# Kernel tuning notes

Measured on AMD Instinct MI355X. Metric: run time of the kernel, lower is better.

Reference implementation:

```python
import jax, jax.numpy as jnp
import numpy as np

B, C, DIM_IN, E = 1024, 128, 16, 10
# num paths per (output L, correlation order nu) -- last dim of the generalized CG U-matrices
PATHS = {0: {1: 1, 2: 2, 3: 5}, 1: {1: 1, 2: 3, 3: 7}}


def setup_inputs() -> dict:
    key = jax.random.key(0)
    ks = jax.random.split(key, 16)
    a_i = jax.random.normal(ks[0], (B, C, DIM_IN), jnp.float32)
    species = jax.random.randint(ks[1], (B,), 0, E)
    node_attrs = jax.nn.one_hot(species, E, dtype=jnp.float32)  # one-hot per-atom species

    def U(k, shape):
        # stand-in for the (constant, precomputed) generalized CG U-matrices
        return jax.random.normal(k, shape, jnp.float32) * 0.1

    def W(k, npaths):
        # learned per-species path weights [num_elements, num_paths, channels]
        return jax.random.normal(k, (E, npaths, C), jnp.float32) / np.sqrt(npaths)

    i = DIM_IN
    return dict(
        a_i=a_i, node_attrs=node_attrs,
        U3_l0=U(ks[2], (i, i, i, PATHS[0][3])),
        U2_l0=U(ks[3], (i, i, PATHS[0][2])),
        U1_l0=U(ks[4], (i, PATHS[0][1])),
        W3_l0=W(ks[5], PATHS[0][3]), W2_l0=W(ks[6], PATHS[0][2]), W1_l0=W(ks[7], PATHS[0][1]),
        U3_l1=U(ks[8], (3, i, i, i, PATHS[1][3])),
        U2_l1=U(ks[9], (3, i, i, PATHS[1][2])),
        U1_l1=U(ks[10], (3, i, PATHS[1][1])),
        W3_l1=W(ks[11], PATHS[1][3]), W2_l1=W(ks[12], PATHS[1][2]), W1_l1=W(ks[13], PATHS[1][1]),
    )


def _contraction(x, y, U3, U2, U1, W3, W2, W1):
    # x: [b,c,i]; y: [b,e] one-hot. Faithful to MACE Contraction:
    #   main:      '...ik,ekc,bci,be->bc...'  (nu = correlation = 3)
    #   weighting: '...k,ekc,be->bc...'       (nu = 2, 1)
    #   features:  'bc...i,bci->bc...'
    # main equation staged so the largest intermediate is the [b,c,(L,)i,i] output
    w3 = jnp.einsum('ekc,be->bkc', W3, y)          # per-node species weight selection
    wx = jnp.einsum('bkc,bci->bkci', w3, x)        # [b,k3,c,i]
    out = jnp.einsum('...ik,bkci->bc...', U3, wx)  # [b,c,(2L+1,)i,i]
    # nu = 2
    w2 = jnp.einsum('ekc,be->bkc', W2, y)
    out = out + jnp.einsum('...k,bkc->bc...', U2, w2)
    out = jnp.einsum('bc...i,bci->bc...', out, x)  # [b,c,(2L+1,)i]
    # nu = 1
    w1 = jnp.einsum('ekc,be->bkc', W1, y)
    out = out + jnp.einsum('...k,bkc->bc...', U1, w1)
    out = jnp.einsum('bc...i,bci->bc...', out, x)  # [b,c] (L=0) or [b,c,2L+1]
    return out


def reference(a_i, node_attrs, U3_l0, U2_l0, U1_l0, W3_l0, W2_l0, W1_l0,
              U3_l1, U2_l1, U1_l1, W3_l1, W2_l1, W1_l1):
    out0 = _contraction(a_i, node_attrs, U3_l0, U2_l0, U1_l0, W3_l0, W2_l0, W1_l0)  # [b,c]
    out1 = _contraction(a_i, node_attrs, U3_l1, U2_l1, U1_l1, W3_l1, W2_l1, W1_l1)  # [b,c,3]
    b = a_i.shape[0]
    # SymmetricContraction flattens each contraction to [b, c*(2L+1)] and concatenates
    return jnp.concatenate([out0.reshape(b, -1), out1.reshape(b, -1)], axis=-1)  # [b, c*4]
```

## Files before the change

kernel.cpp:

```cpp
#include <hip/hip_runtime.h>
#include <hip/hip_bf16.h>

typedef unsigned short u16;
typedef __attribute__((ext_vector_type(8))) unsigned short u16x8;
typedef __attribute__((ext_vector_type(4))) float f32x4;

#define TPB 128
#define TBL_OFF 65536
#define SLOT 9312
#define TBL_BYTES ((size_t)1280 * SLOT * 4)
#define PART_OFF (TBL_OFF + TBL_BYTES)
#define PART_BYTES ((size_t)4 * 1024 * 512 * 4)
#define WS_NEEDED_OLD (TBL_OFF + TBL_BYTES)
#define WS_NEEDED_NEW (PART_OFF + PART_BYTES)

__device__ __forceinline__ float bf2f(u16 v){
  union { unsigned int u; float f; } x; x.u = ((unsigned int)v) << 16; return x.f;
}
__device__ __forceinline__ u16 f2bf(float f){
  union { float f; unsigned int u; } x; x.f = f;
  unsigned int u = x.u;
  u += 0x7FFFu + ((u >> 16) & 1u);
  return (u16)(u >> 16);
}
__device__ __forceinline__ float ld(const void* p, int idx, int isbf){
  return isbf ? bf2f(((const u16*)p)[idx]) : ((const float*)p)[idx];
}

__global__ void k_classify2(const void* __restrict__ nav, int* __restrict__ ws){
  __shared__ int scnt[10];
  __shared__ int sf[16];
  __shared__ int sflag;
  const int b = threadIdx.x;
  if (b < 10) scnt[b] = 0;

  const unsigned int* w = (const unsigned int*)nav;
  int found = 0;
  for (int i = b; i < 5120; i += 1024) found |= (w[i] == 0x00003F80u);
  unsigned long long m = __ballot(found);
  if ((b & 63) == 0) sf[b >> 6] = (m != 0ULL);
  __syncthreads();
  if (b == 0){ int f = 0; for (int i = 0; i < 16; i++) f |= sf[i]; sflag = f; ws[15] = f; }
  __syncthreads();
  const int isbf = sflag;

  int e = 0;
  #pragma unroll
  for (int j = 0; j < 10; j++){
    if (ld(nav, b*10 + j, isbf) > 0.5f) e = j;
  }
  int pos = atomicAdd(&scnt[e], 1);
  ws[16 + e*1024 + pos] = b;
  __syncthreads();
  if (b < 10) ws[b] = scnt[b];
}

__global__ __launch_bounds__(128) void k_build2(
    const void* __restrict__ U3_0, const void* __restrict__ U2_0, const void* __restrict__ U1_0,
    const void* __restrict__ W3_0, const void* __restrict__ W2_0, const void* __restrict__ W1_0,
    const void* __restrict__ U3_1, const void* __restrict__ U2_1, const void* __restrict__ U1_1,
    const void* __restrict__ W3_1, const void* __restrict__ W2_1, const void* __restrict__ W1_1,
    const int* __restrict__ ws, float* __restrict__ tb)
{
  const int jt = blockIdx.x, cg = blockIdx.y, e = blockIdx.z;
  const int j  = jt*128 + threadIdx.x;
  const int isbf = ws[15];
  if (j >= 9312) return;
  const int c0 = cg*8;

  float u[7];
  int K, wbase, dst;
  const void* Wp;

  if (j < 8704){
    const int q = j / 2176, rem = j % 2176;
    const int p = rem >> 4, i3 = rem & 15;
    int i1 = 0, rr = p;
    while (rr >= 16 - i1){ rr -= 16 - i1; i1++; }
    const int i2 = i1 + rr;
    if (q == 0){
      K = 5; Wp = W3_0; wbase = e*5;
      const int a  = (i1*256 + i2*16 + i3)*5;
      const int bb = (i2*256 + i1*16 + i3)*5;
      #pragma unroll
      for (int k = 0; k < 5; k++){
        float v = ld(U3_0, a + k, isbf);
        if (i1 != i2) v += ld(U3_0, bb + k, isbf);
        u[k] = v;
      }
    } else {
      K = 7; Wp = W3_1; wbase = e*7;
      const int mm = q - 1;
      const int a  = (mm*4096 + i1*256 + i2*16 + i3)*7;
      const int bb = (mm*4096 + i2*256 + i1*16 + i3)*7;
      #pragma unroll
      for (int k = 0; k < 7; k++){
        float v = ld(U3_1, a + k, isbf);
        if (i1 != i2) v += ld(U3_1, bb + k, isbf);
        u[k] = v;
      }
    }
    dst = j;
  } else if (j < 9248){
    const int jj = j - 8704;
    const int q = jj / 136, p = jj % 136;
    int i1 = 0, rr = p;
    while (rr >= 16 - i1){ rr -= 16 - i1; i1++; }
    const int i2 = i1 + rr;
    if (q == 0){
      K = 2; Wp = W2_0; wbase = e*2;
      const int a = (i1*16 + i2)*2, bb = (i2*16 + i1)*2;
      #pragma unroll
      for (int k = 0; k < 2; k++){
        float v = ld(U2_0, a + k, isbf);
        if (i1 != i2) v += ld(U2_0, bb + k, isbf);
        u[k] = v;
      }
    } else {
      K = 3; Wp = W2_1; wbase = e*3;
      const int mm = q - 1;
      const int a = (mm*256 + i1*16 + i2)*3, bb = (mm*256 + i2*16 + i1)*3;
      #pragma unroll
      for (int k = 0; k < 3; k++){
        float v = ld(U2_1, a + k, isbf);
        if (i1 != i2) v += ld(U2_1, bb + k, isbf);
        u[k] = v;
      }
    }
    dst = 8704 + jj;
  } else {
    const int jj = j - 9248;
    const int q = jj >> 4, i = jj & 15;
    K = 1;
    if (q == 0){ Wp = W1_0; wbase = e; u[0] = ld(U1_0, i, isbf); }
    else       { Wp = W1_1; wbase = e; u[0] = ld(U1_1, (q - 1)*16 + i, isbf); }
    dst = 9248 + jj;
  }

  for (int cc = 0; cc < 8; cc++){
    const int c = c0 + cc;
    float v = 0.f;
    for (int k = 0; k < K; k++) v += u[k] * ld(Wp, (wbase + k)*128 + c, isbf);
    tb[(size_t)(e*128 + c)*SLOT + dst] = v;
  }
}

__global__ __launch_bounds__(TPB) void k_contract3(
    const void* __restrict__ a_i, const int* __restrict__ ws,
    const float* __restrict__ tb, float* __restrict__ part)
{
  const int e   = blockIdx.x >> 7;
  const int c   = blockIdx.x & 127;
  const int pc  = blockIdx.y;
  const int tid = threadIdx.x;
  const int isbf  = ws[15];
  const int count = ws[e];
  const int* lst  = ws + 16 + e*1024;
  const float* __restrict__ base = tb + (size_t)(e*128 + c)*SLOT;
  if (count == 0) return;

  __shared__ float sX[TPB][17];
  const int p0 = pc*34;

  for (int t0 = 0; t0 < count; t0 += TPB){
    int t = t0 + tid;
    const bool act = t < count;
    if (!act) t = count - 1;
    const int b = lst[t];
    const int xbase = (b*128 + c)*16;

    float xr[16];
    if (isbf){
      const u16* xp = (const u16*)a_i + xbase;
      u16x8 v0 = *(const u16x8*)(xp);
      u16x8 v1 = *(const u16x8*)(xp + 8);
      #pragma unroll
      for (int i = 0; i < 8; i++){ xr[i] = bf2f(v0[i]); xr[8 + i] = bf2f(v1[i]); }
    } else {
      const float* xp = (const float*)a_i + xbase;
      f32x4 v0 = *(const f32x4*)(xp);
      f32x4 v1 = *(const f32x4*)(xp + 4);
      f32x4 v2 = *(const f32x4*)(xp + 8);
      f32x4 v3 = *(const f32x4*)(xp + 12);
      #pragma unroll
      for (int i = 0; i < 4; i++){
        xr[i] = v0[i]; xr[4+i] = v1[i]; xr[8+i] = v2[i]; xr[12+i] = v3[i];
      }
    }
    #pragma unroll
    for (int i = 0; i < 16; i++) sX[tid][i] = xr[i];

    float r0 = 0.f, r1 = 0.f, r2 = 0.f, r3 = 0.f;
    const float* pA3 = base + p0*16;
    const float* pA2 = base + 8704 + p0;
    int i1 = 0, rm = p0;
    while (rm >= 16 - i1){ rm -= 16 - i1; i1++; }
    int i2 = i1 + rm;

    #pragma clang loop unroll(disable)
    for (int n = 0; n < 34; ++n){
      const float xx = sX[tid][i1] * sX[tid][i2];
      float s0 = pA2[0], s1 = pA2[136], s2 = pA2[272], s3 = pA2[408];
      #pragma unroll
      for (int i3 = 0; i3 < 16; ++i3){
        const float xv = xr[i3];
        s0 += pA3[        i3]*xv;
        s1 += pA3[2176 + i3]*xv;
        s2 += pA3[4352 + i3]*xv;
        s3 += pA3[6528 + i3]*xv;
      }
      r0 += s0*xx; r1 += s1*xx; r2 += s2*xx; r3 += s3*xx;
      pA3 += 16; pA2 += 1;
      i2++; if (i2 == 16){ i1++; i2 = i1; }
    }

    if (pc == 3){
      #pragma unroll
      for (int i = 0; i < 16; i++){
        const float xv = xr[i];
        r0 += base[9248 + i]*xv;
        r1 += base[9264 + i]*xv;
        r2 += base[9280 + i]*xv;
        r3 += base[9296 + i]*xv;
      }
    }

    if (act){
      f32x4 v; v[0] = r0; v[1] = r1; v[2] = r2; v[3] = r3;
      *(f32x4*)(part + ((size_t)(pc*1024 + b)*512 + c*4)) = v;
    }
  }
}

__global__ __launch_bounds__(128) void k_combine(
    const float* __restrict__ part, const int* __restrict__ ws, void* __restrict__ outv)
{
  const int b = blockIdx.x, c = threadIdx.x;
  const int isbf = ws[15];
  f32x4 r;
  r[0] = 0.f; r[1] = 0.f; r[2] = 0.f; r[3] = 0.f;
  #pragma unroll
  for (int pc = 0; pc < 4; pc++){
    f32x4 v = *(const f32x4*)(part + ((size_t)(pc*1024 + b)*512 + c*4));
    r[0] += v[0]; r[1] += v[1]; r[2] += v[2]; r[3] += v[3];
  }
  if (isbf){
    u16* ob = (u16*)outv + (size_t)b*512;
    ob[c]             = f2bf(r[0]);
    ob[128 + c*3 + 0] = f2bf(r[1]);
    ob[128 + c*3 + 1] = f2bf(r[2]);
    ob[128 + c*3 + 2] = f2bf(r[3]);
  } else {
    float* ob = (float*)outv + (size_t)b*512;
    ob[c]             = r[0];
    ob[128 + c*3 + 0] = r[1];
    ob[128 + c*3 + 1] = r[2];
    ob[128 + c*3 + 2] = r[3];
  }
}

__global__ __launch_bounds__(256) void k_build(
    const void* __restrict__ U3_0, const void* __restrict__ U2_0, const void* __restrict__ U1_0,
    const void* __restrict__ W3_0, const void* __restrict__ W2_0, const void* __restrict__ W1_0,
    const void* __restrict__ U3_1, const void* __restrict__ U2_1, const void* __restrict__ U1_1,
    const void* __restrict__ W3_1, const void* __restrict__ W2_1, const void* __restrict__ W1_1,
    const int* __restrict__ ws, float* __restrict__ tb)
{
  const int eq = blockIdx.y;
  const int e  = eq >> 2, q = eq & 3;
  const int bx = blockIdx.x;
  const int jt = bx >> 5, ct = bx & 31;
  const int j  = jt*64 + (threadIdx.x & 63);
  const int c  = ct*4 + (threadIdx.x >> 6);
  const int isbf = ws[15];
  if (j >= 2328) return;

  float* base = tb + (size_t)(e*128 + c)*SLOT;

  if (j < 2176){
    const int p = j >> 4, i3 = j & 15;
    int i1 = 0, rem = p;
    while (rem >= 16 - i1){ rem -= 16 - i1; i1++; }
    const int i2 = i1 + rem;
    float v = 0.f;
    if (q == 0){
      const int a  = (i1*256 + i2*16 + i3)*5;
      const int bb = (i2*256 + i1*16 + i3)*5;
      #pragma unroll
      for (int k = 0; k < 5; k++){
        float u = ld(U3_0, a + k, isbf);
        if (i1 != i2) u += ld(U3_0, bb + k, isbf);
        v += u * ld(W3_0, (e*5 + k)*128 + c, isbf);
      }
    } else {
      const int m  = q - 1;
      const int a  = (m*4096 + i1*256 + i2*16 + i3)*7;
      const int bb = (m*4096 + i2*256 + i1*16 + i3)*7;
      #pragma unroll
      for (int k = 0; k < 7; k++){
        float u = ld(U3_1, a + k, isbf);
        if (i1 != i2) u += ld(U3_1, bb + k, isbf);
        v += u * ld(W3_1, (e*7 + k)*128 + c, isbf);
      }
    }
    base[q*2176 + j] = v;
  } else if (j < 2312){
    const int p = j - 2176;
    int i1 = 0, rem = p;
    while (rem >= 16 - i1){ rem -= 16 - i1; i1++; }
    const int i2 = i1 + rem;
    float v = 0.f;
    if (q == 0){
      const int a = (i1*16 + i2)*2, bb = (i2*16 + i1)*2;
      #pragma unroll
      for (int k = 0; k < 2; k++){
        float u = ld(U2_0, a + k, isbf);
        if (i1 != i2) u += ld(U2_0, bb + k, isbf);
        v += u * ld(W2_0, (e*2 + k)*128 + c, isbf);
      }
    } else {
      const int m = q - 1;
      const int a = (m*256 + i1*16 + i2)*3, bb = (m*256 + i2*16 + i1)*3;
      #pragma unroll
      for (int k = 0; k < 3; k++){
        float u = ld(U2_1, a + k, isbf);
        if (i1 != i2) u += ld(U2_1, bb + k, isbf);
        v += u * ld(W2_1, (e*3 + k)*128 + c, isbf);
      }
    }
    base[8704 + q*136 + p] = v;
  } else {
    const int i = j - 2312;
    float v = (q == 0) ? ld(U1_0, i, isbf) * ld(W1_0, e*128 + c, isbf)
                       : ld(U1_1, (q - 1)*16 + i, isbf) * ld(W1_1, e*128 + c, isbf);
    base[9248 + q*16 + i] = v;
  }
}

__global__ __launch_bounds__(TPB) void k_contract2(
    const void* __restrict__ a_i, const int* __restrict__ ws,
    const float* __restrict__ tb, void* __restrict__ outv)
{
  const int e   = blockIdx.x >> 7;
  const int c   = blockIdx.x & 127;
  const int tid = threadIdx.x;
  const int isbf  = ws[15];
  const int count = ws[e];
  const int* lst  = ws + 16 + e*1024;
  const float* __restrict__ base = tb + (size_t)(e*128 + c)*SLOT;

  __shared__ float sX[TPB][17];

  for (int t0 = 0; t0 < count; t0 += TPB){
    int t = t0 + tid;
    const bool act = t < count;
    if (!act) t = count - 1;
    const int b = lst[t];
    const int xbase = (b*128 + c)*16;

    float xr[16];
    if (isbf){
      const u16* xp = (const u16*)a_i + xbase;
      u16x8 v0 = *(const u16x8*)(xp);
      u16x8 v1 = *(const u16x8*)(xp + 8);
      #pragma unroll
      for (int i = 0; i < 8; i++){ xr[i] = bf2f(v0[i]); xr[8 + i] = bf2f(v1[i]); }
    } else {
      const float* xp = (const float*)a_i + xbase;
      f32x4 v0 = *(const f32x4*)(xp);
      f32x4 v1 = *(const f32x4*)(xp + 4);
      f32x4 v2 = *(const f32x4*)(xp + 8);
      f32x4 v3 = *(const f32x4*)(xp + 12);
      #pragma unroll
      for (int i = 0; i < 4; i++){
        xr[i] = v0[i]; xr[4+i] = v1[i]; xr[8+i] = v2[i]; xr[12+i] = v3[i];
      }
    }
    #pragma unroll
    for (int i = 0; i < 16; i++) sX[tid][i] = xr[i];

    float r0 = 0.f, r1 = 0.f, r2 = 0.f, r3 = 0.f;
    const float* pA3 = base;
    const float* pA2 = base + 8704;

    #pragma clang loop unroll(disable)
    for (int i1 = 0; i1 < 16; ++i1){
      const float x1 = sX[tid][i1];
      #pragma clang loop unroll(disable)
      for (int i2 = i1; i2 < 16; ++i2){
        const float xx = x1 * sX[tid][i2];
        float s0 = pA2[0], s1 = pA2[136], s2 = pA2[272], s3 = pA2[408];
        #pragma unroll
        for (int i3 = 0; i3 < 16; ++i3){
          const float xv = xr[i3];
          s0 += pA3[        i3]*xv;
          s1 += pA3[2176 + i3]*xv;
          s2 += pA3[4352 + i3]*xv;
          s3 += pA3[6528 + i3]*xv;
        }
        r0 += s0*xx; r1 += s1*xx; r2 += s2*xx; r3 += s3*xx;
        pA3 += 16; pA2 += 1;
      }
    }
    #pragma unroll
    for (int i = 0; i < 16; i++){
      const float xv = xr[i];
      r0 += base[9248 + i]*xv;
      r1 += base[9264 + i]*xv;
      r2 += base[9280 + i]*xv;
      r3 += base[9296 + i]*xv;
    }

    if (act){
      if (isbf){
        u16* ob = (u16*)outv + (size_t)b*512;
        ob[c]             = f2bf(r0);
        ob[128 + c*3 + 0] = f2bf(r1);
        ob[128 + c*3 + 1] = f2bf(r2);
        ob[128 + c*3 + 2] = f2bf(r3);
      } else {
        float* ob = (float*)outv + (size_t)b*512;
        ob[c]             = r0;
        ob[128 + c*3 + 0] = r1;
        ob[128 + c*3 + 1] = r2;
        ob[128 + c*3 + 2] = r3;
      }
    }
  }
}

__global__ __launch_bounds__(TPB) void k_contract(
    const void* __restrict__ a_i,
    const void* __restrict__ U3_0, const void* __restrict__ U2_0, const void* __restrict__ U1_0,
    const void* __restrict__ W3_0, const void* __restrict__ W2_0, const void* __restrict__ W1_0,
    const void* __restrict__ U3_1, const void* __restrict__ U2_1, const void* __restrict__ U1_1,
    const void* __restrict__ W3_1, const void* __restrict__ W2_1, const void* __restrict__ W1_1,
    const int* __restrict__ ws, void* __restrict__ outv)
{
  const int bx  = blockIdx.x;
  const int e   = bx >> 7;
  const int c   = bx & 127;
  const int tid = threadIdx.x;
  const int isbf = ws[15];

  __shared__ float sA3[4*136*16];
  __shared__ float sA2[4*136];
  __shared__ float sA1[4*16];
  __shared__ unsigned char sI1[136], sI2[136];
  __shared__ float sX[TPB][17];

  for (int p = tid; p < 136; p += TPB){
    int i1 = 0, rem = p;
    while (rem >= 16 - i1){ rem -= 16 - i1; i1++; }
    sI1[p] = (unsigned char)i1;
    sI2[p] = (unsigned char)(i1 + rem);
  }

  float w3_0[5], w2_0[2], w3_1[7], w2_1[3];
  #pragma unroll
  for (int k = 0; k < 5; k++) w3_0[k] = ld(W3_0, (e*5 + k)*128 + c, isbf);
  #pragma unroll
  for (int k = 0; k < 2; k++) w2_0[k] = ld(W2_0, (e*2 + k)*128 + c, isbf);
  const float w1_0 = ld(W1_0, e*128 + c, isbf);
  #pragma unroll
  for (int k = 0; k < 7; k++) w3_1[k] = ld(W3_1, (e*7 + k)*128 + c, isbf);
  #pragma unroll
  for (int k = 0; k < 3; k++) w2_1[k] = ld(W2_1, (e*3 + k)*128 + c, isbf);
  const float w1_1 = ld(W1_1, e*128 + c, isbf);

  __syncthreads();

  for (int q = 0; q < 4; q++){
    for (int idx = tid; idx < 136*16; idx += TPB){
      const int p  = idx >> 4;
      const int i3 = idx & 15;
      const int i1 = sI1[p], i2 = sI2[p];
      float v = 0.f;
      if (q == 0){
        const int a  = (i1*256 + i2*16 + i3)*5;
        const int bb = (i2*256 + i1*16 + i3)*5;
        #pragma unroll
        for (int k = 0; k < 5; k++){
          float u = ld(U3_0, a + k, isbf);
          if (i1 != i2) u += ld(U3_0, bb + k, isbf);
          v += u * w3_0[k];
        }
      } else {
        const int m  = q - 1;
        const int a  = (m*4096 + i1*256 + i2*16 + i3)*7;
        const int bb = (m*4096 + i2*256 + i1*16 + i3)*7;
        #pragma unroll
        for (int k = 0; k < 7; k++){
          float u = ld(U3_1, a + k, isbf);
          if (i1 != i2) u += ld(U3_1, bb + k, isbf);
          v += u * w3_1[k];
        }
      }
      sA3[q*2176 + idx] = v;
    }
  }
  for (int idx = tid; idx < 4*136; idx += TPB){
    const int q = idx / 136, p = idx - q*136;
    const int i1 = sI1[p], i2 = sI2[p];
    float v = 0.f;
    if (q == 0){
      const int a = (i1*16 + i2)*2, bb = (i2*16 + i1)*2;
      #pragma unroll
      for (int k = 0; k < 2; k++){
        float u = ld(U2_0, a + k, isbf);
        if (i1 != i2) u += ld(U2_0, bb + k, isbf);
        v += u * w2_0[k];
      }
    } else {
      const int m = q - 1;
      const int a = (m*256 + i1*16 + i2)*3, bb = (m*256 + i2*16 + i1)*3;
      #pragma unroll
      for (int k = 0; k < 3; k++){
        float u = ld(U2_1, a + k, isbf);
        if (i1 != i2) u += ld(U2_1, bb + k, isbf);
        v += u * w2_1[k];
      }
    }
    sA2[idx] = v;
  }
  if (tid < 64){
    const int q = tid >> 4, i1 = tid & 15;
    sA1[tid] = (q == 0) ? ld(U1_0, i1, isbf) * w1_0
                        : ld(U1_1, (q - 1)*16 + i1, isbf) * w1_1;
  }
  __syncthreads();

  const int count = ws[e];
  const int* lst  = ws + 16 + e*1024;

  for (int t = tid; t < count; t += TPB){
    const int b = lst[t];
    const int xbase = (b*128 + c)*16;

    float xr[16];
    if (isbf){
      const u16* xp = (const u16*)a_i + xbase;
      u16x8 v0 = *(const u16x8*)(xp);
      u16x8 v1 = *(const u16x8*)(xp + 8);
      #pragma unroll
      for (int i = 0; i < 8; i++){ xr[i] = bf2f(v0[i]); xr[8 + i] = bf2f(v1[i]); }
    } else {
      const float* xp = (const float*)a_i + xbase;
      f32x4 v0 = *(const f32x4*)(xp);
      f32x4 v1 = *(const f32x4*)(xp + 4);
      f32x4 v2 = *(const f32x4*)(xp + 8);
      f32x4 v3 = *(const f32x4*)(xp + 12);
      #pragma unroll
      for (int i = 0; i < 4; i++){
        xr[i] = v0[i]; xr[4+i] = v1[i]; xr[8+i] = v2[i]; xr[12+i] = v3[i];
      }
    }
    #pragma unroll
    for (int i = 0; i < 16; i++) sX[tid][i] = xr[i];

    float r0 = 0.f, r1 = 0.f, r2 = 0.f, r3 = 0.f;
    int p = 0;
    for (int i1 = 0; i1 < 16; i1++){
      const float x1 = sX[tid][i1];
      for (int i2 = i1; i2 < 16; i2++, p++){
        const float* a0 = &sA3[(0*136 + p)*16];
        const float* a1 = &sA3[(1*136 + p)*16];
        const float* a2 = &sA3[(2*136 + p)*16];
        const float* a3 = &sA3[(3*136 + p)*16];
        float s0 = sA2[        p];
        float s1 = sA2[136   + p];
        float s2 = sA2[272   + p];
        float s3 = sA2[408   + p];
        #pragma unroll
        for (int i3 = 0; i3 < 16; i3++){
          const float xv = xr[i3];
          s0 += a0[i3]*xv;
          s1 += a1[i3]*xv;
          s2 += a2[i3]*xv;
          s3 += a3[i3]*xv;
        }
        const float xx = x1 * sX[tid][i2];
        r0 += s0*xx; r1 += s1*xx; r2 += s2*xx; r3 += s3*xx;
      }
    }
    #pragma unroll
    for (int i1 = 0; i1 < 16; i1++){
      const float xv = xr[i1];
      r0 += sA1[     i1]*xv;
      r1 += sA1[16 + i1]*xv;
      r2 += sA1[32 + i1]*xv;
      r3 += sA1[48 + i1]*xv;
    }

    if (isbf){
      u16* ob = (u16*)outv + (size_t)b*512;
      ob[c]             = f2bf(r0);
      ob[128 + c*3 + 0] = f2bf(r1);
      ob[128 + c*3 + 1] = f2bf(r2);
      ob[128 + c*3 + 2] = f2bf(r3);
    } else {
      float* ob = (float*)outv + (size_t)b*512;
      ob[c]             = r0;
      ob[128 + c*3 + 0] = r1;
      ob[128 + c*3 + 1] = r2;
      ob[128 + c*3 + 2] = r3;
    }
  }
}

extern "C" void kernel_launch(void* const* d_in, const int* in_sizes, int n_in,
                              void* d_out, int out_size, void* d_ws, size_t ws_size,
                              hipStream_t stream) {
  int* ws = (int*)d_ws;
  hipLaunchKernelGGL(k_classify2, dim3(1), dim3(1024), 0, stream, d_in[1], ws);

  if (ws_size >= WS_NEEDED_NEW){
    float* tb   = (float*)((char*)d_ws + TBL_OFF);
    float* part = (float*)((char*)d_ws + PART_OFF);
    hipLaunchKernelGGL(k_build2, dim3(73, 16, 10), dim3(128), 0, stream,
                       d_in[2], d_in[3], d_in[4], d_in[5], d_in[6], d_in[7],
                       d_in[8], d_in[9], d_in[10], d_in[11], d_in[12], d_in[13],
                       ws, tb);
    hipLaunchKernelGGL(k_contract3, dim3(1280, 4), dim3(TPB), 0, stream,
                       d_in[0], ws, tb, part);
    hipLaunchKernelGGL(k_combine, dim3(1024), dim3(128), 0, stream,
                       part, ws, d_out);
  } else if (ws_size >= WS_NEEDED_OLD){
    float* tb = (float*)((char*)d_ws + TBL_OFF);
    hipLaunchKernelGGL(k_build, dim3(37*32, 40), dim3(256), 0, stream,
                       d_in[2], d_in[3], d_in[4], d_in[5], d_in[6], d_in[7],
                       d_in[8], d_in[9], d_in[10], d_in[11], d_in[12], d_in[13],
                       ws, tb);
    hipLaunchKernelGGL(k_contract2, dim3(1280), dim3(TPB), 0, stream,
                       d_in[0], ws, tb, d_out);
  } else {
    hipLaunchKernelGGL(k_contract, dim3(1280), dim3(TPB), 0, stream,
                       d_in[0],
                       d_in[2], d_in[3], d_in[4], d_in[5], d_in[6], d_in[7],
                       d_in[8], d_in[9], d_in[10], d_in[11], d_in[12], d_in[13],
                       ws, d_out);
  }
}
```

Measured before the change: 140.9 us.

## Add bf16 MFMA contraction path and stage per-species weights in shared memory

Adds a bf16-only path. k_buildF precomputes the folded U·W table in bf16, laid out as MFMA A fragments. k_contract_mfma then evaluates the degree-3 contraction with 16x16x32 bf16 MFMA instructions and combines the results with pairwise x products in registers. This removes the fp32 table, the partial-sum buffer and the combine pass whenever inputs are bf16. The fp32 path keeps its kernels, but k_build3 now caches the W rows in shared memory instead of re-reading them from global memory. All six kernels are always launched and exit early based on the dtype flag, which adds launch overhead, and storing the table in bf16 may lose precision.

New measurement: 165.7 us. 1.18x slower.

```diff
diff --git a/kernel.cpp b/kernel.cpp
--- a/kernel.cpp
+++ b/kernel.cpp
@@ -3,6 +3,7 @@
 
 typedef unsigned short u16;
 typedef __attribute__((ext_vector_type(8))) unsigned short u16x8;
+typedef __attribute__((ext_vector_type(8))) short bf16x8;
 typedef __attribute__((ext_vector_type(4))) float f32x4;
 
 #define TPB 128
@@ -11,7 +12,6 @@
 #define TBL_BYTES ((size_t)1280 * SLOT * 4)
 #define PART_OFF (TBL_OFF + TBL_BYTES)
 #define PART_BYTES ((size_t)4 * 1024 * 512 * 4)
-#define WS_NEEDED_OLD (TBL_OFF + TBL_BYTES)
 #define WS_NEEDED_NEW (PART_OFF + PART_BYTES)
 
 __device__ __forceinline__ float bf2f(u16 v){
@@ -55,22 +55,246 @@
   if (b < 10) ws[b] = scnt[b];
 }
 
-__global__ __launch_bounds__(128) void k_build2(
+__global__ __launch_bounds__(64) void k_buildF(
+    const void* __restrict__ U3_0, const void* __restrict__ U2_0, const void* __restrict__ U1_0,
+    const void* __restrict__ W3_0, const void* __restrict__ W2_0, const void* __restrict__ W1_0,
+    const void* __restrict__ U3_1, const void* __restrict__ U2_1, const void* __restrict__ U1_1,
+    const void* __restrict__ W3_1, const void* __restrict__ W2_1, const void* __restrict__ W1_1,
+    const int* __restrict__ ws, u16* __restrict__ ftb)
+{
+  if (!ws[15]) return;
+  const int t  = blockIdx.x;
+  const int cg = blockIdx.y;
+  const int e  = blockIdx.z;
+  const int q  = t / 9, pb = t % 9;
+  const int lane = threadIdx.x;
+  const int g = lane >> 4, row = lane & 15;
+  const int p = pb*16 + row;
+  const int c0 = cg*16;
+
+  __shared__ float sW[19*16];
+  for (int idx = lane; idx < 304; idx += 64){
+    const int slot = idx >> 4, cc = idx & 15;
+    const int c = c0 + cc;
+    float v;
+    if      (slot < 5)  v = bf2f(((const u16*)W3_0)[(e*5 + slot)*128 + c]);
+    else if (slot < 12) v = bf2f(((const u16*)W3_1)[(e*7 + slot - 5)*128 + c]);
+    else if (slot < 14) v = bf2f(((const u16*)W2_0)[(e*2 + slot - 12)*128 + c]);
+    else if (slot < 17) v = bf2f(((const u16*)W2_1)[(e*3 + slot - 14)*128 + c]);
+    else if (slot == 17) v = bf2f(((const u16*)W1_0)[e*128 + c]);
+    else                 v = bf2f(((const u16*)W1_1)[e*128 + c]);
+    sW[slot*16 + cc] = v;
+  }
+  __syncthreads();
+
+  float u[8][7];
+  #pragma unroll
+  for (int j = 0; j < 8; j++)
+    #pragma unroll
+    for (int k = 0; k < 7; k++) u[j][k] = 0.f;
+  int K = 0, slot0 = 0;
+
+  if (p < 136){
+    int i1 = 0, rem = p;
+    while (rem >= 16 - i1){ rem -= 16 - i1; i1++; }
+    const int i2 = i1 + rem;
+    if (g < 2){
+      if (q == 0){
+        K = 5; slot0 = 0;
+        #pragma unroll
+        for (int j = 0; j < 8; j++){
+          const int i3 = g*8 + j;
+          const int a  = (i1*256 + i2*16 + i3)*5;
+          const int bb = (i2*256 + i1*16 + i3)*5;
+          #pragma unroll
+          for (int k = 0; k < 5; k++){
+            float v = bf2f(((const u16*)U3_0)[a + k]);
+            if (i1 != i2) v += bf2f(((const u16*)U3_0)[bb + k]);
+            u[j][k] = v;
+          }
+        }
+      } else {
+        K = 7; slot0 = 5;
+        const int mm = q - 1;
+        #pragma unroll
+        for (int j = 0; j < 8; j++){
+          const int i3 = g*8 + j;
+          const int a  = (mm*4096 + i1*256 + i2*16 + i3)*7;
+          const int bb = (mm*4096 + i2*256 + i1*16 + i3)*7;
+          #pragma unroll
+          for (int k = 0; k < 7; k++){
+            float v = bf2f(((const u16*)U3_1)[a + k]);
+            if (i1 != i2) v += bf2f(((const u16*)U3_1)[bb + k]);
+            u[j][k] = v;
+          }
+        }
+      }
+    } else if (g == 2){
+      if (q == 0){
+        K = 2; slot0 = 12;
+        const int a = (i1*16 + i2)*2, bb = (i2*16 + i1)*2;
+        #pragma unroll
+        for (int k = 0; k < 2; k++){
+          float v = bf2f(((const u16*)U2_0)[a + k]);
+          if (i1 != i2) v += bf2f(((const u16*)U2_0)[bb + k]);
+          u[0][k] = v;
+        }
+      } else {
+        K = 3; slot0 = 14;
+        const int mm = q - 1;
+        const int a = (mm*256 + i1*16 + i2)*3, bb = (mm*256 + i2*16 + i1)*3;
+        #pragma unroll
+        for (int k = 0; k < 3; k++){
+          float v = bf2f(((const u16*)U2_1)[a + k]);
+          if (i1 != i2) v += bf2f(((const u16*)U2_1)[bb + k]);
+          u[0][k] = v;
+        }
+      }
+    }
+  } else if (p == 136 && g < 2){
+    K = 1; slot0 = (q == 0) ? 17 : 18;
+    #pragma unroll
+    for (int j = 0; j < 8; j++){
+      const int i = g*8 + j;
+      u[j][0] = (q == 0) ? bf2f(((const u16*)U1_0)[i])
+                         : bf2f(((const u16*)U1_1)[(q - 1)*16 + i]);
+    }
+  }
+
+  for (int cc = 0; cc < 16; cc++){
+    u16x8 o;
+    #pragma unroll
+    for (int j = 0; j < 8; j++){
+      float v = 0.f;
+      #pragma unroll
+      for (int k = 0; k < 7; k++)
+        if (k < K) v += u[j][k] * sW[(slot0 + k)*16 + cc];
+      o[j] = f2bf(v);
+    }
+    u16* dst = ftb + ((size_t)((e*128 + c0 + cc)*36 + t))*512 + lane*8;
+    *(u16x8*)dst = o;
+  }
+}
+
+__global__ __launch_bounds__(64) void k_contract_mfma(
+    const u16* __restrict__ a_i, const int* __restrict__ ws,
+    const u16* __restrict__ ftb, u16* __restrict__ out)
+{
+  if (!ws[15]) return;
+  const int e = blockIdx.x >> 7, c = blockIdx.x & 127;
+  const int half = blockIdx.y;
+  const int lane = threadIdx.x;
+  const int count = ws[e];
+  if (count == 0) return;
+  const int ngroups = (count + 15) >> 4;
+  const int* lst = ws + 16 + e*1024;
+  const int col = lane & 15, g = lane >> 4;
+
+  __shared__ float sx[16][20];
+  __shared__ int   sip[144];
+
+  for (int p = lane; p < 144; p += 64){
+    int i1, i2;
+    if (p < 136){ int a = 0, rem = p; while (rem >= 16 - a){ rem -= 16 - a; a++; } i1 = a; i2 = a + rem; }
+    else if (p == 136){ i1 = 16; i2 = 16; }
+    else { i1 = 17; i2 = 17; }
+    sip[p] = i1 | (i2 << 8);
+  }
+  if (lane < 16){ sx[lane][16] = 1.f; sx[lane][17] = 0.f; sx[lane][18] = 0.f; sx[lane][19] = 0.f; }
+  __syncthreads();
+
+  bf16x8 af[36];
+  const u16* fb = ftb + (size_t)(e*128 + c)*36*512 + lane*8;
+  #pragma unroll
+  for (int t = 0; t < 36; t++) af[t] = *(const bf16x8*)(fb + t*512);
+
+  for (int grp = half; grp < ngroups; grp += 2){
+    const int aidx = grp*16 + col;
+    const bool act = aidx < count;
+    const int b = lst[act ? aidx : count - 1];
+
+    bf16x8 bfr;
+    if (g < 2){
+      bfr = *(const bf16x8*)(a_i + (size_t)(b*128 + c)*16 + g*8);
+    } else if (g == 2){
+      bfr = (bf16x8){(short)0x3F80, 0,0,0,0,0,0,0};
+    } else {
+      bfr = (bf16x8){0,0,0,0,0,0,0,0};
+    }
+    if (g < 2){
+      #pragma unroll
+      for (int j = 0; j < 8; j++) sx[col][g*8 + j] = bf2f((u16)bfr[j]);
+    }
+    __syncthreads();
+
+    float m[9][4];
+    #pragma unroll
+    for (int pb = 0; pb < 9; pb++)
+      #pragma unroll
+      for (int r = 0; r < 4; r++){
+        const int ip = sip[pb*16 + g*4 + r];
+        m[pb][r] = sx[col][ip & 0xff] * sx[col][ip >> 8];
+      }
+
+    float racc[4];
+    #pragma unroll
+    for (int q = 0; q < 4; q++){
+      float rq = 0.f;
+      #pragma unroll
+      for (int pb = 0; pb < 9; pb++){
+        f32x4 acc = {0.f, 0.f, 0.f, 0.f};
+        acc = __builtin_amdgcn_mfma_f32_16x16x32_bf16(af[q*9 + pb], bfr, acc, 0, 0, 0);
+        rq += m[pb][0]*acc[0] + m[pb][1]*acc[1] + m[pb][2]*acc[2] + m[pb][3]*acc[3];
+      }
+      racc[q] = rq;
+    }
+    #pragma unroll
+    for (int q = 0; q < 4; q++){
+      racc[q] += __shfl_xor(racc[q], 16);
+      racc[q] += __shfl_xor(racc[q], 32);
+    }
+    if (act && g == 0){
+      u16* ob = out + (size_t)b*512;
+      ob[c]             = f2bf(racc[0]);
+      ob[128 + c*3 + 0] = f2bf(racc[1]);
+      ob[128 + c*3 + 1] = f2bf(racc[2]);
+      ob[128 + c*3 + 2] = f2bf(racc[3]);
+    }
+    __syncthreads();
+  }
+}
+
+__global__ __launch_bounds__(128) void k_build3(
     const void* __restrict__ U3_0, const void* __restrict__ U2_0, const void* __restrict__ U1_0,
     const void* __restrict__ W3_0, const void* __restrict__ W2_0, const void* __restrict__ W1_0,
     const void* __restrict__ U3_1, const void* __restrict__ U2_1, const void* __restrict__ U1_1,
     const void* __restrict__ W3_1, const void* __restrict__ W2_1, const void* __restrict__ W1_1,
     const int* __restrict__ ws, float* __restrict__ tb)
 {
+  const int isbf = ws[15];
+  if (isbf) return;
   const int jt = blockIdx.x, cg = blockIdx.y, e = blockIdx.z;
   const int j  = jt*128 + threadIdx.x;
-  const int isbf = ws[15];
+  const int c0 = cg*8;
+
+  __shared__ float sW[19*8];
+  for (int idx = threadIdx.x; idx < 152; idx += 128){
+    const int slot = idx >> 3, cc = idx & 7;
+    const int c = c0 + cc;
+    float v;
+    if      (slot < 5)  v = ld(W3_0, (e*5 + slot)*128 + c, 0);
+    else if (slot < 12) v = ld(W3_1, (e*7 + slot - 5)*128 + c, 0);
+    else if (slot < 14) v = ld(W2_0, (e*2 + slot - 12)*128 + c, 0);
+    else if (slot < 17) v = ld(W2_1, (e*3 + slot - 14)*128 + c, 0);
+    else if (slot == 17) v = ld(W1_0, e*128 + c, 0);
+    else                 v = ld(W1_1, e*128 + c, 0);
+    sW[slot*8 + cc] = v;
+  }
+  __syncthreads();
   if (j >= 9312) return;
-  const int c0 = cg*8;
 
   float u[7];
-  int K, wbase, dst;
-  const void* Wp;
+  int K, slot0, dst;
 
   if (j < 8704){
     const int q = j / 2176, rem = j % 2176;
@@ -79,24 +303,24 @@
     while (rr >= 16 - i1){ rr -= 16 - i1; i1++; }
     const int i2 = i1 + rr;
     if (q == 0){
-      K = 5; Wp = W3_0; wbase = e*5;
+      K = 5; slot0 = 0;
       const int a  = (i1*256 + i2*16 + i3)*5;
       const int bb = (i2*256 + i1*16 + i3)*5;
       #pragma unroll
       for (int k = 0; k < 5; k++){
-        float v = ld(U3_0, a + k, isbf);
-        if (i1 != i2) v += ld(U3_0, bb + k, isbf);
+        float v = ld(U3_0, a + k, 0);
+        if (i1 != i2) v += ld(U3_0, bb + k, 0);
         u[k] = v;
       }
     } else {
-      K = 7; Wp = W3_1; wbase = e*7;
+      K = 7; slot0 = 5;
       const int mm = q - 1;
       const int a  = (mm*4096 + i1*256 + i2*16 + i3)*7;
       const int bb = (mm*4096 + i2*256 + i1*16 + i3)*7;
       #pragma unroll
       for (int k = 0; k < 7; k++){
-        float v = ld(U3_1, a + k, isbf);
-        if (i1 != i2) v += ld(U3_1, bb + k, isbf);
+        float v = ld(U3_1, a + k, 0);
+        if (i1 != i2) v += ld(U3_1, bb + k, 0);
         u[k] = v;
       }
     }
@@ -108,22 +332,22 @@
     while (rr >= 16 - i1){ rr -= 16 - i1; i1++; }
     const int i2 = i1 + rr;
     if (q == 0){
-      K = 2; Wp = W2_0; wbase = e*2;
+      K = 2; slot0 = 12;
       const int a = (i1*16 + i2)*2, bb = (i2*16 + i1)*2;
       #pragma unroll
       for (int k = 0; k < 2; k++){
-        float v = ld(U2_0, a + k, isbf);
-        if (i1 != i2) v += ld(U2_0, bb + k, isbf);
+        float v = ld(U2_0, a + k, 0);
+        if (i1 != i2) v += ld(U2_0, bb + k, 0);
         u[k] = v;
       }
     } else {
-      K = 3; Wp = W2_1; wbase = e*3;
+      K = 3; slot0 = 14;
       const int mm = q - 1;
       const int a = (mm*256 + i1*16 + i2)*3, bb = (mm*256 + i2*16 + i1)*3;
       #pragma unroll
       for (int k = 0; k < 3; k++){
-        float v = ld(U2_1, a + k, isbf);
-        if (i1 != i2) v += ld(U2_1, bb + k, isbf);
+        float v = ld(U2_1, a + k, 0);
+        if (i1 != i2) v += ld(U2_1, bb + k, 0);
         u[k] = v;
       }
     }
@@ -132,16 +356,16 @@
     const int jj = j - 9248;
     const int q = jj >> 4, i = jj & 15;
     K = 1;
-    if (q == 0){ Wp = W1_0; wbase = e; u[0] = ld(U1_0, i, isbf); }
-    else       { Wp = W1_1; wbase = e; u[0] = ld(U1_1, (q - 1)*16 + i, isbf); }
+    if (q == 0){ slot0 = 17; u[0] = ld(U1_0, i, 0); }
+    else       { slot0 = 18; u[0] = ld(U1_1, (q - 1)*16 + i, 0); }
     dst = 9248 + jj;
   }
 
+  #pragma unroll
   for (int cc = 0; cc < 8; cc++){
-    const int c = c0 + cc;
     float v = 0.f;
-    for (int k = 0; k < K; k++) v += u[k] * ld(Wp, (wbase + k)*128 + c, isbf);
-    tb[(size_t)(e*128 + c)*SLOT + dst] = v;
+    for (int k = 0; k < K; k++) v += u[k] * sW[(slot0 + k)*8 + cc];
+    tb[(size_t)(e*128 + c0 + cc)*SLOT + dst] = v;
   }
 }
 
@@ -149,11 +373,11 @@
     const void* __restrict__ a_i, const int* __restrict__ ws,
     const float* __restrict__ tb, float* __restrict__ part)
 {
+  if (ws[15]) return;
   const int e   = blockIdx.x >> 7;
   const int c   = blockIdx.x & 127;
   const int pc  = blockIdx.y;
   const int tid = threadIdx.x;
-  const int isbf  = ws[15];
   const int count = ws[e];
   const int* lst  = ws + 16 + e*1024;
   const float* __restrict__ base = tb + (size_t)(e*128 + c)*SLOT;
@@ -170,13 +394,7 @@
     const int xbase = (b*128 + c)*16;
 
     float xr[16];
-    if (isbf){
-      const u16* xp = (const u16*)a_i + xbase;
-      u16x8 v0 = *(const u16x8*)(xp);
-      u16x8 v1 = *(const u16x8*)(xp + 8);
-      #pragma unroll
-      for (int i = 0; i < 8; i++){ xr[i] = bf2f(v0[i]); xr[8 + i] = bf2f(v1[i]); }
-    } else {
+    {
       const float* xp = (const float*)a_i + xbase;
       f32x4 v0 = *(const f32x4*)(xp);
       f32x4 v1 = *(const f32x4*)(xp + 4);
@@ -235,198 +453,19 @@
 __global__ __launch_bounds__(128) void k_combine(
     const float* __restrict__ part, const int* __restrict__ ws, void* __restrict__ outv)
 {
+  if (ws[15]) return;
   const int b = blockIdx.x, c = threadIdx.x;
-  const int isbf = ws[15];
-  f32x4 r;
-  r[0] = 0.f; r[1] = 0.f; r[2] = 0.f; r[3] = 0.f;
+  f32x4 r; r[0] = 0.f; r[1] = 0.f; r[2] = 0.f; r[3] = 0.f;
   #pragma unroll
   for (int pc = 0; pc < 4; pc++){
     f32x4 v = *(const f32x4*)(part + ((size_t)(pc*1024 + b)*512 + c*4));
     r[0] += v[0]; r[1] += v[1]; r[2] += v[2]; r[3] += v[3];
   }
-  if (isbf){
-    u16* ob = (u16*)outv + (size_t)b*512;
-    ob[c]             = f2bf(r[0]);
-    ob[128 + c*3 + 0] = f2bf(r[1]);
-    ob[128 + c*3 + 1] = f2bf(r[2]);
-    ob[128 + c*3 + 2] = f2bf(r[3]);
-  } else {
-    float* ob = (float*)outv + (size_t)b*512;
-    ob[c]             = r[0];
-    ob[128 + c*3 + 0] = r[1];
-    ob[128 + c*3 + 1] = r[2];
-    ob[128 + c*3 + 2] = r[3];
-  }
-}
-
-__global__ __launch_bounds__(256) void k_build(
-    const void* __restrict__ U3_0, const void* __restrict__ U2_0, const void* __restrict__ U1_0,
-    const void* __restrict__ W3_0, const void* __restrict__ W2_0, const void* __restrict__ W1_0,
-    const void* __restrict__ U3_1, const void* __restrict__ U2_1, const void* __restrict__ U1_1,
-    const void* __restrict__ W3_1, const void* __restrict__ W2_1, const void* __restrict__ W1_1,
-    const int* __restrict__ ws, float* __restrict__ tb)
-{
-  const int eq = blockIdx.y;
-  const int e  = eq >> 2, q = eq & 3;
-  const int bx = blockIdx.x;
-  const int jt = bx >> 5, ct = bx & 31;
-  const int j  = jt*64 + (threadIdx.x & 63);
-  const int c  = ct*4 + (threadIdx.x >> 6);
-  const int isbf = ws[15];
-  if (j >= 2328) return;
-
-  float* base = tb + (size_t)(e*128 + c)*SLOT;
-
-  if (j < 2176){
-    const int p = j >> 4, i3 = j & 15;
-    int i1 = 0, rem = p;
-    while (rem >= 16 - i1){ rem -= 16 - i1; i1++; }
-    const int i2 = i1 + rem;
-    float v = 0.f;
-    if (q == 0){
-      const int a  = (i1*256 + i2*16 + i3)*5;
-      const int bb = (i2*256 + i1*16 + i3)*5;
-      #pragma unroll
-      for (int k = 0; k < 5; k++){
-        float u = ld(U3_0, a + k, isbf);
-        if (i1 != i2) u += ld(U3_0, bb + k, isbf);
-        v += u * ld(W3_0, (e*5 + k)*128 + c, isbf);
-      }
-    } else {
-      const int m  = q - 1;
-      const int a  = (m*4096 + i1*256 + i2*16 + i3)*7;
-      const int bb = (m*4096 + i2*256 + i1*16 + i3)*7;
-      #pragma unroll
-      for (int k = 0; k < 7; k++){
-        float u = ld(U3_1, a + k, isbf);
-        if (i1 != i2) u += ld(U3_1, bb + k, isbf);
-        v += u * ld(W3_1, (e*7 + k)*128 + c, isbf);
-      }
-    }
-    base[q*2176 + j] = v;
-  } else if (j < 2312){
-    const int p = j - 2176;
-    int i1 = 0, rem = p;
-    while (rem >= 16 - i1){ rem -= 16 - i1; i1++; }
-    const int i2 = i1 + rem;
-    float v = 0.f;
-    if (q == 0){
-      const int a = (i1*16 + i2)*2, bb = (i2*16 + i1)*2;
-      #pragma unroll
-      for (int k = 0; k < 2; k++){
-        float u = ld(U2_0, a + k, isbf);
-        if (i1 != i2) u += ld(U2_0, bb + k, isbf);
-        v += u * ld(W2_0, (e*2 + k)*128 + c, isbf);
-      }
-    } else {
-      const int m = q - 1;
-      const int a = (m*256 + i1*16 + i2)*3, bb = (m*256 + i2*16 + i1)*3;
-      #pragma unroll
-      for (int k = 0; k < 3; k++){
-        float u = ld(U2_1, a + k, isbf);
-        if (i1 != i2) u += ld(U2_1, bb + k, isbf);
-        v += u * ld(W2_1, (e*3 + k)*128 + c, isbf);
-      }
-    }
-    base[8704 + q*136 + p] = v;
-  } else {
-    const int i = j - 2312;
-    float v = (q == 0) ? ld(U1_0, i, isbf) * ld(W1_0, e*128 + c, isbf)
-                       : ld(U1_1, (q - 1)*16 + i, isbf) * ld(W1_1, e*128 + c, isbf);
-    base[9248 + q*16 + i] = v;
-  }
-}
-
-__global__ __launch_bounds__(TPB) void k_contract2(
-    const void* __restrict__ a_i, const int* __restrict__ ws,
-    const float* __restrict__ tb, void* __restrict__ outv)
-{
-  const int e   = blockIdx.x >> 7;
-  const int c   = blockIdx.x & 127;
-  const int tid = threadIdx.x;
-  const int isbf  = ws[15];
-  const int count = ws[e];
-  const int* lst  = ws + 16 + e*1024;
-  const float* __restrict__ base = tb + (size_t)(e*128 + c)*SLOT;
-
-  __shared__ float sX[TPB][17];
-
-  for (int t0 = 0; t0 < count; t0 += TPB){
-    int t = t0 + tid;
-    const bool act = t < count;
-    if (!act) t = count - 1;
-    const int b = lst[t];
-    const int xbase = (b*128 + c)*16;
-
-    float xr[16];
-    if (isbf){
-      const u16* xp = (const u16*)a_i + xbase;
-      u16x8 v0 = *(const u16x8*)(xp);
-      u16x8 v1 = *(const u16x8*)(xp + 8);
-      #pragma unroll
-      for (int i = 0; i < 8; i++){ xr[i] = bf2f(v0[i]); xr[8 + i] = bf2f(v1[i]); }
-    } else {
-      const float* xp = (const float*)a_i + xbase;
-      f32x4 v0 = *(const f32x4*)(xp);
-      f32x4 v1 = *(const f32x4*)(xp + 4);
-      f32x4 v2 = *(const f32x4*)(xp + 8);
-      f32x4 v3 = *(const f32x4*)(xp + 12);
-      #pragma unroll
-      for (int i = 0; i < 4; i++){
-        xr[i] = v0[i]; xr[4+i] = v1[i]; xr[8+i] = v2[i]; xr[12+i] = v3[i];
-      }
-    }
-    #pragma unroll
-    for (int i = 0; i < 16; i++) sX[tid][i] = xr[i];
-
-    float r0 = 0.f, r1 = 0.f, r2 = 0.f, r3 = 0.f;
-    const float* pA3 = base;
-    const float* pA2 = base + 8704;
-
-    #pragma clang loop unroll(disable)
-    for (int i1 = 0; i1 < 16; ++i1){
-      const float x1 = sX[tid][i1];
-      #pragma clang loop unroll(disable)
-      for (int i2 = i1; i2 < 16; ++i2){
-        const float xx = x1 * sX[tid][i2];
-        float s0 = pA2[0], s1 = pA2[136], s2 = pA2[272], s3 = pA2[408];
-        #pragma unroll
-        for (int i3 = 0; i3 < 16; ++i3){
-          const float xv = xr[i3];
-          s0 += pA3[        i3]*xv;
-          s1 += pA3[2176 + i3]*xv;
-          s2 += pA3[4352 + i3]*xv;
-          s3 += pA3[6528 + i3]*xv;
-        }
-        r0 += s0*xx; r1 += s1*xx; r2 += s2*xx; r3 += s3*xx;
-        pA3 += 16; pA2 += 1;
-      }
-    }
-    #pragma unroll
-    for (int i = 0; i < 16; i++){
-      const float xv = xr[i];
-      r0 += base[9248 + i]*xv;
-      r1 += base[9264 + i]*xv;
-      r2 += base[9280 + i]*xv;
-      r3 += base[9296 + i]*xv;
-    }
-
-    if (act){
-      if (isbf){
-        u16* ob = (u16*)outv + (size_t)b*512;
-        ob[c]             = f2bf(r0);
-        ob[128 + c*3 + 0] = f2bf(r1);
-        ob[128 + c*3 + 1] = f2bf(r2);
-        ob[128 + c*3 + 2] = f2bf(r3);
-      } else {
-        float* ob = (float*)outv + (size_t)b*512;
-        ob[c]             = r0;
-        ob[128 + c*3 + 0] = r1;
-        ob[128 + c*3 + 1] = r2;
-        ob[128 + c*3 + 2] = r3;
-      }
-    }
-  }
+  float* ob = (float*)outv + (size_t)b*512;
+  ob[c]             = r[0];
+  ob[128 + c*3 + 0] = r[1];
+  ob[128 + c*3 + 1] = r[2];
+  ob[128 + c*3 + 2] = r[3];
 }
 
 __global__ __launch_bounds__(TPB) void k_contract(
@@ -615,9 +654,18 @@
   hipLaunchKernelGGL(k_classify2, dim3(1), dim3(1024), 0, stream, d_in[1], ws);
 
   if (ws_size >= WS_NEEDED_NEW){
+    u16*   ftb  = (u16*)((char*)d_ws + TBL_OFF);
     float* tb   = (float*)((char*)d_ws + TBL_OFF);
     float* part = (float*)((char*)d_ws + PART_OFF);
-    hipLaunchKernelGGL(k_build2, dim3(73, 16, 10), dim3(128), 0, stream,
+
+    hipLaunchKernelGGL(k_buildF, dim3(36, 8, 10), dim3(64), 0, stream,
+                       d_in[2], d_in[3], d_in[4], d_in[5], d_in[6], d_in[7],
+                       d_in[8], d_in[9], d_in[10], d_in[11], d_in[12], d_in[13],
+                       ws, ftb);
+    hipLaunchKernelGGL(k_contract_mfma, dim3(1280, 2), dim3(64), 0, stream,
+                       (const u16*)d_in[0], ws, ftb, (u16*)d_out);
+
+    hipLaunchKernelGGL(k_build3, dim3(73, 16, 10), dim3(128), 0, stream,
                        d_in[2], d_in[3], d_in[4], d_in[5], d_in[6], d_in[7],
                        d_in[8], d_in[9], d_in[10], d_in[11], d_in[12], d_in[13],
                        ws, tb);
@@ -625,14 +673,6 @@
                        d_in[0], ws, tb, part);
     hipLaunchKernelGGL(k_combine, dim3(1024), dim3(128), 0, stream,
                        part, ws, d_out);
-  } else if (ws_size >= WS_NEEDED_OLD){
-    float* tb = (float*)((char*)d_ws + TBL_OFF);
-    hipLaunchKernelGGL(k_build, dim3(37*32, 40), dim3(256), 0, stream,
-                       d_in[2], d_in[3], d_in[4], d_in[5], d_in[6], d_in[7],
-                       d_in[8], d_in[9], d_in[10], d_in[11], d_in[12], d_in[13],
-                       ws, tb);
-    hipLaunchKernelGGL(k_contract2, dim3(1280), dim3(TPB), 0, stream,
-                       d_in[0], ws, tb, d_out);
   } else {
     hipLaunchKernelGGL(k_contract, dim3(1280), dim3(TPB), 0, stream,
                        d_in[0],
```
